# Optimization experiments

Hardware: AMD Instinct MI355X
Metric: run time of the kernel (lower is better)

## Reference

```python
import jax, jax.numpy as jnp
import numpy as np

B, S, D, H = 2, 2048, 1024, 16
DK = D // H


def setup_inputs() -> dict:
    key = jax.random.key(0)
    ks = jax.random.split(key, 11)
    s = 1.0 / np.sqrt(D)
    inp = {
        "q": jax.random.normal(ks[0], (B, S, D), jnp.float32),
        "k": jax.random.normal(ks[1], (B, S, D), jnp.float32),
        "v": jax.random.normal(ks[2], (B, S, D), jnp.float32),
        # causal (lower-triangular) decoder mask, broadcast over batch & heads
        "mask": jnp.tril(jnp.ones((S, S), jnp.int32))[None, None, :, :],
        "Wq": jax.random.normal(ks[3], (D, D), jnp.float32) * s,
        "bq": jax.random.normal(ks[4], (D,), jnp.float32) * s,
        "Wk": jax.random.normal(ks[5], (D, D), jnp.float32) * s,
        "bk": jax.random.normal(ks[6], (D,), jnp.float32) * s,
        "Wv": jax.random.normal(ks[7], (D, D), jnp.float32) * s,
        "bv": jax.random.normal(ks[8], (D,), jnp.float32) * s,
        "Wo": jax.random.normal(ks[9], (D, D), jnp.float32) * s,
        "bo": jax.random.normal(ks[10], (D,), jnp.float32) * s,
    }
    return inp


def reference(q, k, v, mask, Wq, bq, Wk, bk, Wv, bv, Wo, bo):
    # projections (nn.Linear: x @ W.T + b)
    def proj(x, W, b):
        return (x @ W.T + b).reshape(B, S, H, DK).transpose(0, 2, 1, 3)  # [B,H,S,DK]

    Q = proj(q, Wq, bq)
    K = proj(k, Wk, bk)
    V = proj(v, Wv, bv)

    scores = jnp.einsum("bhsd,bhtd->bhst", Q, K) / jnp.sqrt(jnp.float32(DK))
    scores = jnp.where(mask == 0, jnp.float32(-1e9), scores)
    attn = jax.nn.softmax(scores, axis=-1)  # dropout=0.0 -> identity
    ctx = jnp.einsum("bhst,bhtd->bhsd", attn, V)
    ctx = ctx.transpose(0, 2, 1, 3).reshape(B, S, D)
    return ctx @ Wo.T + bo
```

## Files before the change

### kernel.cpp

```cpp
#include <hip/hip_runtime.h>

typedef __bf16 bf16;
typedef __bf16 bf16x4 __attribute__((ext_vector_type(4)));
typedef __bf16 bf16x8 __attribute__((ext_vector_type(8)));
typedef float floatx4 __attribute__((ext_vector_type(4)));

#define NB 2
#define NS 2048
#define ND 1024
#define NH 16
#define NDK 64
#define NM (NB * NS)

__device__ __forceinline__ void async_cp16(const void* g, void* l) {
  __builtin_amdgcn_global_load_lds(
      (const __attribute__((address_space(1))) void*)g,
      (__attribute__((address_space(3))) void*)l, 16, 0, 0);
}

__device__ __forceinline__ bf16x8 cvt8(const float* p) {
  float4 lo = *(const float4*)p, hi = *(const float4*)(p + 4);
  bf16x8 o;
  o[0] = (bf16)lo.x; o[1] = (bf16)lo.y; o[2] = (bf16)lo.z; o[3] = (bf16)lo.w;
  o[4] = (bf16)hi.x; o[5] = (bf16)hi.y; o[6] = (bf16)hi.z; o[7] = (bf16)hi.w;
  return o;
}

__device__ __forceinline__ void wg_barrier_lds() {
  __asm__ __volatile__("s_waitcnt lgkmcnt(0)" ::: "memory");
  __builtin_amdgcn_s_barrier();
}

__device__ __forceinline__ void tr2(const void* p, bf16x4& lo, bf16x4& hi) {
  asm volatile("ds_read_b64_tr_b16 %0, %2\n\t"
               "ds_read_b64_tr_b16 %1, %2 offset:512"
               : "=&v"(lo), "=&v"(hi)
               : "v"((const __attribute__((address_space(3))) void*)p));
}

struct CvtArgs {
  const float* src[8];
  bf16* dst[8];
  int nblk[8];
  int nseg;
};

__global__ __launch_bounds__(256) void cvt_kernel(CvtArgs a) {
  int b = blockIdx.x, seg = 0;
  while (seg < a.nseg - 1 && b >= a.nblk[seg]) { b -= a.nblk[seg]; ++seg; }
  const size_t idx = ((size_t)b * 256 + threadIdx.x) * 8;
  *(bf16x8*)(a.dst[seg] + idx) = cvt8(a.src[seg] + idx);
}

template <int TM, typename TA, typename TC>
__global__ __launch_bounds__(256) void gemm_dma(
    const TA* __restrict__ A0, const TA* __restrict__ A1, const TA* __restrict__ A2,
    const bf16* __restrict__ W0, const bf16* __restrict__ W1, const bf16* __restrict__ W2,
    const float* __restrict__ bias0, const float* __restrict__ bias1, const float* __restrict__ bias2,
    TC* __restrict__ C0, TC* __restrict__ C1, TC* __restrict__ C2)
{
  const int z = blockIdx.z;
  const TA* A = (z == 0) ? A0 : (z == 1) ? A1 : A2;
  const bf16* W = (z == 0) ? W0 : (z == 1) ? W1 : W2;
  const float* bias = (z == 0) ? bias0 : (z == 1) ? bias1 : bias2;
  TC* C = (z == 0) ? C0 : (z == 1) ? C1 : C2;

  __shared__ bf16 At[TM * 32];
  __shared__ bf16 Bt[128 * 32];

  const int tid = threadIdx.x;
  const int wave = tid >> 6, lane = tid & 63;
  const int q4 = lane >> 4, l15 = lane & 15;
  const int m0 = blockIdx.y * TM, n0 = blockIdx.x * 128;
  constexpr int WM = TM / 2;
  constexpr int MI = WM / 16;
  const int wm = (wave >> 1) * WM, wn = (wave & 1) * 64;

  floatx4 acc[MI][4] = {};

  const bf16* Wg = W + (size_t)(n0 + (lane >> 2)) * ND + (lane & 3) * 8;
  const bf16* Ag = nullptr;
  const float* Af = nullptr;
  const int srow = tid >> 2, sk = (tid & 3) * 8;
  if constexpr (sizeof(TA) == 2)
    Ag = (const bf16*)A + (size_t)(m0 + (lane >> 2)) * ND + (lane & 3) * 8;
  else
    Af = (const float*)A + (size_t)(m0 + srow) * ND + sk;

  for (int k0 = 0; k0 < ND; k0 += 32) {
    bf16x8 a0, a1;
    if constexpr (sizeof(TA) == 4) {
      a0 = cvt8(Af + k0);
      if constexpr (TM == 128) a1 = cvt8(Af + (size_t)64 * ND + k0);
    }
    __syncthreads();
#pragma unroll
    for (int c2 = 0; c2 < 2; ++c2) {
      const int c = wave * 2 + c2;
      async_cp16(Wg + (size_t)c * 16 * ND + k0, &Bt[c * 16 * 32]);
    }
    if constexpr (sizeof(TA) == 2) {
#pragma unroll
      for (int c2 = 0; c2 < TM / 64; ++c2) {
        const int c = wave * (TM / 64) + c2;
        async_cp16(Ag + (size_t)c * 16 * ND + k0, &At[c * 16 * 32]);
      }
    } else {
      *(bf16x8*)&At[srow * 32 + sk] = a0;
      if constexpr (TM == 128) *(bf16x8*)&At[(srow + 64) * 32 + sk] = a1;
    }
    __syncthreads();

    bf16x8 af[MI], bfr[4];
#pragma unroll
    for (int i = 0; i < MI; ++i)
      af[i] = *(const bf16x8*)&At[(wm + i * 16 + l15) * 32 + q4 * 8];
#pragma unroll
    for (int j = 0; j < 4; ++j)
      bfr[j] = *(const bf16x8*)&Bt[(wn + j * 16 + l15) * 32 + q4 * 8];
#pragma unroll
    for (int i = 0; i < MI; ++i)
#pragma unroll
      for (int j = 0; j < 4; ++j)
        acc[i][j] = __builtin_amdgcn_mfma_f32_16x16x32_bf16(af[i], bfr[j], acc[i][j], 0, 0, 0);
  }

#pragma unroll
  for (int j = 0; j < 4; ++j) {
    const int col = n0 + wn + j * 16 + l15;
    const float bv = bias[col];
#pragma unroll
    for (int i = 0; i < MI; ++i) {
      const int rowb = m0 + wm + i * 16 + q4 * 4;
#pragma unroll
      for (int r = 0; r < 4; ++r)
        C[(size_t)(rowb + r) * ND + col] = (TC)(acc[i][j][r] + bv);
    }
  }
}

#define NEGBIG (-1e30f)
#define LDP 72

__global__ __launch_bounds__(256) void attn_kernel(
    const bf16* __restrict__ Q, const bf16* __restrict__ K,
    const bf16* __restrict__ V, bf16* __restrict__ O)
{
  __shared__ bf16 vt[2][4096];
  __shared__ bf16 pbuf[4][16 * LDP];

  const int bx = blockIdx.x;
  const int h = blockIdx.y, b = blockIdx.z;
  const int tid = threadIdx.x, wave = tid >> 6, lane = tid & 63;
  const int q4 = lane >> 4, l15 = lane & 15;

  const bf16* kp = K + ((size_t)(b * NS) + l15) * ND + h * NDK + q4 * 8;

  const int sg0 = wave * 8 + (lane >> 3);
  const int sg1 = 32 + sg0;
  const int vs0 = ((sg0 >> 2) << 2) + ((lane & 7) >> 1);
  const int vs1 = ((sg1 >> 2) << 2) + ((lane & 7) >> 1);
  const int vd0 = (sg0 & 3) * 16 + (lane & 1) * 8;
  const int vd1 = (sg1 & 3) * 16 + (lane & 1) * 8;
  const bf16* vp0 = V + ((size_t)(b * NS) + vs0) * ND + h * NDK + vd0;
  const bf16* vp1 = V + ((size_t)(b * NS) + vs1) * ND + h * NDK + vd1;

  const int trb = (lane >> 4) * 512 + l15 * 4;

  bf16x8 qf[2];
  floatx4 oacc[4];
  float psum[4];
  bf16x8 kA[8], kB[8];

  auto ldK = [&](int j, bf16x8 (&kk)[8]) {
    const bf16* p = kp + (size_t)j * (64 * ND);
#pragma unroll
    for (int nf = 0; nf < 4; ++nf)
#pragma unroll
      for (int t = 0; t < 2; ++t)
        kk[nf * 2 + t] = *(const bf16x8*)(p + (size_t)nf * 16 * ND + t * 32);
  };
  auto stageV = [&](int j, int buf) {
    const size_t off = (size_t)j * (64 * ND);
    async_cp16(vp0 + off, &vt[buf][wave * 512]);
    async_cp16(vp1 + off, &vt[buf][2048 + wave * 512]);
  };

  auto body = [&](int j, int iq, bf16x8 (&kc)[8], bf16x8 (&kn)[8]) {
    const int cur = j & 1;

    floatx4 sf[4];
    __builtin_amdgcn_s_setprio(1);
#pragma unroll
    for (int nf = 0; nf < 4; ++nf) {
      floatx4 s = {0.f, 0.f, 0.f, 0.f};
      s = __builtin_amdgcn_mfma_f32_16x16x32_bf16(qf[0], kc[nf * 2 + 0], s, 0, 0, 0);
      s = __builtin_amdgcn_mfma_f32_16x16x32_bf16(qf[1], kc[nf * 2 + 1], s, 0, 0, 0);
      sf[nf] = s;
    }
    __builtin_amdgcn_s_setprio(0);

    wg_barrier_lds();

    if (j < iq) {
      stageV(j + 1, cur ^ 1);
      asm volatile("" ::: "memory");
      ldK(j + 1, kn);
    }

    if (j == iq) {
#pragma unroll
      for (int nf = 0; nf < 4; ++nf) {
        const int kc2 = nf * 16 + l15;
#pragma unroll
        for (int r = 0; r < 4; ++r)
          if (kc2 > wave * 16 + q4 * 4 + r) sf[nf][r] = NEGBIG;
      }
    }

    bf16x4 vlo[4][2], vhi[4][2];
#pragma unroll
    for (int nf = 0; nf < 4; ++nf)
#pragma unroll
      for (int t = 0; t < 2; ++t)
        tr2(&vt[cur][t * 2048 + nf * 64 + trb], vlo[nf][t], vhi[nf][t]);

#pragma unroll
    for (int nf = 0; nf < 4; ++nf)
#pragma unroll
      for (int r = 0; r < 4; ++r) {
        const float pv = exp2f(sf[nf][r]);
        psum[r] += pv;
        pbuf[wave][(q4 * 4 + r) * LDP + nf * 16 + l15] = (bf16)pv;
      }

    asm volatile("s_waitcnt lgkmcnt(0)" ::: "memory");
    __builtin_amdgcn_sched_barrier(0);

    bf16x8 pa0 = *(const bf16x8*)&pbuf[wave][l15 * LDP + q4 * 8];
    bf16x8 pa1 = *(const bf16x8*)&pbuf[wave][l15 * LDP + 32 + q4 * 8];

    __builtin_amdgcn_s_setprio(1);
#pragma unroll
    for (int nf = 0; nf < 4; ++nf) {
      bf16x8 vb0 = __builtin_shufflevector(vlo[nf][0], vhi[nf][0], 0, 1, 2, 3, 4, 5, 6, 7);
      bf16x8 vb1 = __builtin_shufflevector(vlo[nf][1], vhi[nf][1], 0, 1, 2, 3, 4, 5, 6, 7);
      oacc[nf] = __builtin_amdgcn_mfma_f32_16x16x32_bf16(pa0, vb0, oacc[nf], 0, 0, 0);
      oacc[nf] = __builtin_amdgcn_mfma_f32_16x16x32_bf16(pa1, vb1, oacc[nf], 0, 0, 0);
    }
    __builtin_amdgcn_s_setprio(0);
  };

  for (int ph = 0; ph < 2; ++ph) {
    const int iq = ph ? (31 - bx) : bx;
    __syncthreads();

    const size_t qrow0 = (size_t)(b * NS + iq * 64 + wave * 16 + l15);
#pragma unroll
    for (int t = 0; t < 2; ++t) {
      bf16x8 tmp = *(const bf16x8*)(Q + qrow0 * ND + h * NDK + t * 32 + q4 * 8);
#pragma unroll
      for (int e = 0; e < 8; ++e) qf[t][e] = (bf16)((float)tmp[e] * 0.180336880f);
    }

#pragma unroll
    for (int nf = 0; nf < 4; ++nf) oacc[nf] = floatx4{0.f, 0.f, 0.f, 0.f};
#pragma unroll
    for (int r = 0; r < 4; ++r) psum[r] = 0.f;

    stageV(0, 0);
    asm volatile("" ::: "memory");
    ldK(0, kA);
    for (int j = 0; j <= iq; ++j) {
      if ((j & 1) == 0) body(j, iq, kA, kB);
      else              body(j, iq, kB, kA);
    }

#pragma unroll
    for (int r = 0; r < 4; ++r)
#pragma unroll
      for (int off = 1; off < 16; off <<= 1) psum[r] += __shfl_xor(psum[r], off, 16);

#pragma unroll
    for (int nf = 0; nf < 4; ++nf)
#pragma unroll
      for (int r = 0; r < 4; ++r) {
        const int qrow = iq * 64 + wave * 16 + q4 * 4 + r;
        O[(size_t)(b * NS + qrow) * ND + h * NDK + nf * 16 + l15] =
            (bf16)(oacc[nf][r] / psum[r]);
      }
  }
}

extern "C" void kernel_launch(void* const* d_in, const int* in_sizes, int n_in,
                              void* d_out, int out_size, void* d_ws, size_t ws_size,
                              hipStream_t stream) {
  const float* q  = (const float*)d_in[0];
  const float* k  = (const float*)d_in[1];
  const float* v  = (const float*)d_in[2];
  const float* Wq = (const float*)d_in[4];
  const float* bq = (const float*)d_in[5];
  const float* Wk = (const float*)d_in[6];
  const float* bk = (const float*)d_in[7];
  const float* Wv = (const float*)d_in[8];
  const float* bv = (const float*)d_in[9];
  const float* Wo = (const float*)d_in[10];
  const float* bo = (const float*)d_in[11];
  float* out = (float*)d_out;
  char* w = (char*)d_ws;

  const dim3 attn_grid(NS / 128, NH, NB);

  if (ws_size >= (size_t)56 << 20) {
    bf16* xq = (bf16*)(w);
    bf16* xk = (bf16*)(w + ((size_t)8 << 20));
    bf16* xv = (bf16*)(w + ((size_t)16 << 20));
    bf16* wq = (bf16*)(w + ((size_t)24 << 20));
    bf16* wk = (bf16*)(w + ((size_t)26 << 20));
    bf16* wv = (bf16*)(w + ((size_t)28 << 20));
    bf16* wo = (bf16*)(w + ((size_t)30 << 20));
    bf16* Qb = (bf16*)(w + ((size_t)32 << 20));
    bf16* Kb = (bf16*)(w + ((size_t)40 << 20));
    bf16* Vb = (bf16*)(w + ((size_t)48 << 20));
    bf16* Ob = xq;

    CvtArgs ca{};
    const int b4 = (int)((size_t)NM * ND / 2048);
    const int b1 = (int)((size_t)ND * ND / 2048);
    ca.src[0] = q;  ca.dst[0] = xq; ca.nblk[0] = b4;
    ca.src[1] = k;  ca.dst[1] = xk; ca.nblk[1] = b4;
    ca.src[2] = v;  ca.dst[2] = xv; ca.nblk[2] = b4;
    ca.src[3] = Wq; ca.dst[3] = wq; ca.nblk[3] = b1;
    ca.src[4] = Wk; ca.dst[4] = wk; ca.nblk[4] = b1;
    ca.src[5] = Wv; ca.dst[5] = wv; ca.nblk[5] = b1;
    ca.src[6] = Wo; ca.dst[6] = wo; ca.nblk[6] = b1;
    ca.nseg = 7;
    cvt_kernel<<<3 * b4 + 4 * b1, 256, 0, stream>>>(ca);

    gemm_dma<128, bf16, bf16><<<dim3(8, 32, 3), 256, 0, stream>>>(
        xq, xk, xv, wq, wk, wv, bq, bk, bv, Qb, Kb, Vb);
    attn_kernel<<<attn_grid, 256, 0, stream>>>(Qb, Kb, Vb, Ob);
    gemm_dma<64, bf16, float><<<dim3(8, 64, 1), 256, 0, stream>>>(
        Ob, Ob, Ob, wo, wo, wo, bo, bo, bo, out, out, out);
  } else if (ws_size >= (size_t)40 << 20) {
    bf16* wq = (bf16*)(w);
    bf16* wk = (bf16*)(w + ((size_t)2 << 20));
    bf16* wv = (bf16*)(w + ((size_t)4 << 20));
    bf16* wo = (bf16*)(w + ((size_t)6 << 20));
    bf16* Qb = (bf16*)(w + ((size_t)8 << 20));
    bf16* Kb = (bf16*)(w + ((size_t)16 << 20));
    bf16* Vb = (bf16*)(w + ((size_t)24 << 20));
    bf16* Ob = (bf16*)(w + ((size_t)32 << 20));

    CvtArgs ca{};
    const int b1 = (int)((size_t)ND * ND / 2048);
    ca.src[0] = Wq; ca.dst[0] = wq; ca.nblk[0] = b1;
    ca.src[1] = Wk; ca.dst[1] = wk; ca.nblk[1] = b1;
    ca.src[2] = Wv; ca.dst[2] = wv; ca.nblk[2] = b1;
    ca.src[3] = Wo; ca.dst[3] = wo; ca.nblk[3] = b1;
    ca.nseg = 4;
    cvt_kernel<<<4 * b1, 256, 0, stream>>>(ca);

    gemm_dma<128, float, bf16><<<dim3(8, 32, 3), 256, 0, stream>>>(
        q, k, v, wq, wk, wv, bq, bk, bv, Qb, Kb, Vb);
    attn_kernel<<<attn_grid, 256, 0, stream>>>(Qb, Kb, Vb, Ob);
    gemm_dma<64, bf16, float><<<dim3(8, 64, 1), 256, 0, stream>>>(
        Ob, Ob, Ob, wo, wo, wo, bo, bo, bo, out, out, out);
  }
}
```

Before: 260.8 us.

## Split attention key dimension across wave pairs with LDS reduction

```diff
diff --git a/kernel.cpp b/kernel.cpp
--- a/kernel.cpp
+++ b/kernel.cpp
@@ -140,59 +140,56 @@
 }
 
 #define NEGBIG (-1e30f)
-#define LDP 72
-
-__global__ __launch_bounds__(256) void attn_kernel(
+#define LDP2 40
+
+__global__ __launch_bounds__(512) void attn_kernel(
     const bf16* __restrict__ Q, const bf16* __restrict__ K,
     const bf16* __restrict__ V, bf16* __restrict__ O)
 {
   __shared__ bf16 vt[2][4096];
-  __shared__ bf16 pbuf[4][16 * LDP];
+  __shared__ bf16 pbuf[8][16 * LDP2];
+  __shared__ float red[4][64][20];
 
   const int bx = blockIdx.x;
   const int h = blockIdx.y, b = blockIdx.z;
   const int tid = threadIdx.x, wave = tid >> 6, lane = tid & 63;
   const int q4 = lane >> 4, l15 = lane & 15;
-
-  const bf16* kp = K + ((size_t)(b * NS) + l15) * ND + h * NDK + q4 * 8;
+  const int qs = wave >> 1;
+  const int ks = wave & 1;
+
+  const bf16* kp = K + ((size_t)(b * NS) + ks * 32 + l15) * ND + h * NDK + q4 * 8;
 
   const int sg0 = wave * 8 + (lane >> 3);
-  const int sg1 = 32 + sg0;
   const int vs0 = ((sg0 >> 2) << 2) + ((lane & 7) >> 1);
-  const int vs1 = ((sg1 >> 2) << 2) + ((lane & 7) >> 1);
   const int vd0 = (sg0 & 3) * 16 + (lane & 1) * 8;
-  const int vd1 = (sg1 & 3) * 16 + (lane & 1) * 8;
   const bf16* vp0 = V + ((size_t)(b * NS) + vs0) * ND + h * NDK + vd0;
-  const bf16* vp1 = V + ((size_t)(b * NS) + vs1) * ND + h * NDK + vd1;
 
   const int trb = (lane >> 4) * 512 + l15 * 4;
 
   bf16x8 qf[2];
   floatx4 oacc[4];
   float psum[4];
-  bf16x8 kA[8], kB[8];
-
-  auto ldK = [&](int j, bf16x8 (&kk)[8]) {
+  bf16x8 kA[4], kB[4];
+
+  auto ldK = [&](int j, bf16x8 (&kk)[4]) {
     const bf16* p = kp + (size_t)j * (64 * ND);
 #pragma unroll
-    for (int nf = 0; nf < 4; ++nf)
+    for (int nf = 0; nf < 2; ++nf)
 #pragma unroll
       for (int t = 0; t < 2; ++t)
         kk[nf * 2 + t] = *(const bf16x8*)(p + (size_t)nf * 16 * ND + t * 32);
   };
   auto stageV = [&](int j, int buf) {
-    const size_t off = (size_t)j * (64 * ND);
-    async_cp16(vp0 + off, &vt[buf][wave * 512]);
-    async_cp16(vp1 + off, &vt[buf][2048 + wave * 512]);
+    async_cp16(vp0 + (size_t)j * (64 * ND), &vt[buf][wave * 512]);
   };
 
-  auto body = [&](int j, int iq, bf16x8 (&kc)[8], bf16x8 (&kn)[8]) {
+  auto body = [&](int j, int iq, bf16x8 (&kc)[4], bf16x8 (&kn)[4]) {
     const int cur = j & 1;
 
-    floatx4 sf[4];
+    floatx4 sf[2];
     __builtin_amdgcn_s_setprio(1);
 #pragma unroll
-    for (int nf = 0; nf < 4; ++nf) {
+    for (int nf = 0; nf < 2; ++nf) {
       floatx4 s = {0.f, 0.f, 0.f, 0.f};
       s = __builtin_amdgcn_mfma_f32_16x16x32_bf16(qf[0], kc[nf * 2 + 0], s, 0, 0, 0);
       s = __builtin_amdgcn_mfma_f32_16x16x32_bf16(qf[1], kc[nf * 2 + 1], s, 0, 0, 0);
@@ -210,43 +207,38 @@
 
     if (j == iq) {
 #pragma unroll
-      for (int nf = 0; nf < 4; ++nf) {
-        const int kc2 = nf * 16 + l15;
+      for (int nf = 0; nf < 2; ++nf) {
+        const int keyl = ks * 32 + nf * 16 + l15;
 #pragma unroll
         for (int r = 0; r < 4; ++r)
-          if (kc2 > wave * 16 + q4 * 4 + r) sf[nf][r] = NEGBIG;
+          if (keyl > qs * 16 + q4 * 4 + r) sf[nf][r] = NEGBIG;
       }
     }
 
-    bf16x4 vlo[4][2], vhi[4][2];
+    bf16x4 vlo[4], vhi[4];
 #pragma unroll
     for (int nf = 0; nf < 4; ++nf)
-#pragma unroll
-      for (int t = 0; t < 2; ++t)
-        tr2(&vt[cur][t * 2048 + nf * 64 + trb], vlo[nf][t], vhi[nf][t]);
-
-#pragma unroll
-    for (int nf = 0; nf < 4; ++nf)
+      tr2(&vt[cur][ks * 2048 + nf * 64 + trb], vlo[nf], vhi[nf]);
+
+#pragma unroll
+    for (int nf = 0; nf < 2; ++nf)
 #pragma unroll
       for (int r = 0; r < 4; ++r) {
         const float pv = exp2f(sf[nf][r]);
         psum[r] += pv;
-        pbuf[wave][(q4 * 4 + r) * LDP + nf * 16 + l15] = (bf16)pv;
+        pbuf[wave][(q4 * 4 + r) * LDP2 + nf * 16 + l15] = (bf16)pv;
       }
 
     asm volatile("s_waitcnt lgkmcnt(0)" ::: "memory");
     __builtin_amdgcn_sched_barrier(0);
 
-    bf16x8 pa0 = *(const bf16x8*)&pbuf[wave][l15 * LDP + q4 * 8];
-    bf16x8 pa1 = *(const bf16x8*)&pbuf[wave][l15 * LDP + 32 + q4 * 8];
+    bf16x8 pa = *(const bf16x8*)&pbuf[wave][l15 * LDP2 + q4 * 8];
 
     __builtin_amdgcn_s_setprio(1);
 #pragma unroll
     for (int nf = 0; nf < 4; ++nf) {
-      bf16x8 vb0 = __builtin_shufflevector(vlo[nf][0], vhi[nf][0], 0, 1, 2, 3, 4, 5, 6, 7);
-      bf16x8 vb1 = __builtin_shufflevector(vlo[nf][1], vhi[nf][1], 0, 1, 2, 3, 4, 5, 6, 7);
-      oacc[nf] = __builtin_amdgcn_mfma_f32_16x16x32_bf16(pa0, vb0, oacc[nf], 0, 0, 0);
-      oacc[nf] = __builtin_amdgcn_mfma_f32_16x16x32_bf16(pa1, vb1, oacc[nf], 0, 0, 0);
+      bf16x8 vb = __builtin_shufflevector(vlo[nf], vhi[nf], 0, 1, 2, 3, 4, 5, 6, 7);
+      oacc[nf] = __builtin_amdgcn_mfma_f32_16x16x32_bf16(pa, vb, oacc[nf], 0, 0, 0);
     }
     __builtin_amdgcn_s_setprio(0);
   };
@@ -255,7 +247,7 @@
     const int iq = ph ? (31 - bx) : bx;
     __syncthreads();
 
-    const size_t qrow0 = (size_t)(b * NS + iq * 64 + wave * 16 + l15);
+    const size_t qrow0 = (size_t)(b * NS + iq * 64 + qs * 16 + l15);
 #pragma unroll
     for (int t = 0; t < 2; ++t) {
       bf16x8 tmp = *(const bf16x8*)(Q + qrow0 * ND + h * NDK + t * 32 + q4 * 8);
@@ -276,19 +268,35 @@
       else              body(j, iq, kB, kA);
     }
 
-#pragma unroll
-    for (int r = 0; r < 4; ++r)
-#pragma unroll
-      for (int off = 1; off < 16; off <<= 1) psum[r] += __shfl_xor(psum[r], off, 16);
-
-#pragma unroll
-    for (int nf = 0; nf < 4; ++nf)
-#pragma unroll
-      for (int r = 0; r < 4; ++r) {
-        const int qrow = iq * 64 + wave * 16 + q4 * 4 + r;
-        O[(size_t)(b * NS + qrow) * ND + h * NDK + nf * 16 + l15] =
-            (bf16)(oacc[nf][r] / psum[r]);
-      }
+    if (ks == 1) {
+#pragma unroll
+      for (int nf = 0; nf < 4; ++nf)
+        *(floatx4*)&red[qs][lane][nf * 4] = oacc[nf];
+#pragma unroll
+      for (int r = 0; r < 4; ++r) red[qs][lane][16 + r] = psum[r];
+    }
+    __syncthreads();
+    if (ks == 0) {
+#pragma unroll
+      for (int nf = 0; nf < 4; ++nf)
+        oacc[nf] += *(const floatx4*)&red[qs][lane][nf * 4];
+#pragma unroll
+      for (int r = 0; r < 4; ++r) psum[r] += red[qs][lane][16 + r];
+
+#pragma unroll
+      for (int r = 0; r < 4; ++r)
+#pragma unroll
+        for (int off = 1; off < 16; off <<= 1) psum[r] += __shfl_xor(psum[r], off, 16);
+
+#pragma unroll
+      for (int nf = 0; nf < 4; ++nf)
+#pragma unroll
+        for (int r = 0; r < 4; ++r) {
+          const int qrow = iq * 64 + qs * 16 + q4 * 4 + r;
+          O[(size_t)(b * NS + qrow) * ND + h * NDK + nf * 16 + l15] =
+              (bf16)(oacc[nf][r] / psum[r]);
+        }
+    }
   }
 }
 
@@ -339,7 +347,7 @@
 
     gemm_dma<128, bf16, bf16><<<dim3(8, 32, 3), 256, 0, stream>>>(
         xq, xk, xv, wq, wk, wv, bq, bk, bv, Qb, Kb, Vb);
-    attn_kernel<<<attn_grid, 256, 0, stream>>>(Qb, Kb, Vb, Ob);
+    attn_kernel<<<attn_grid, 512, 0, stream>>>(Qb, Kb, Vb, Ob);
     gemm_dma<64, bf16, float><<<dim3(8, 64, 1), 256, 0, stream>>>(
         Ob, Ob, Ob, wo, wo, wo, bo, bo, bo, out, out, out);
   } else if (ws_size >= (size_t)40 << 20) {
@@ -363,7 +371,7 @@
 
     gemm_dma<128, float, bf16><<<dim3(8, 32, 3), 256, 0, stream>>>(
         q, k, v, wq, wk, wv, bq, bk, bv, Qb, Kb, Vb);
-    attn_kernel<<<attn_grid, 256, 0, stream>>>(Qb, Kb, Vb, Ob);
+    attn_kernel<<<attn_grid, 512, 0, stream>>>(Qb, Kb, Vb, Ob);
     gemm_dma<64, bf16, float><<<dim3(8, 64, 1), 256, 0, stream>>>(
         Ob, Ob, Ob, wo, wo, wo, bo, bo, bo, out, out, out);
   }
```

New measurement: 296.0 us. 1.13x slower.
